# Kernel optimization log

Measured on AMD Instinct MI355X. Metric: run time of the kernel, lower is better.

## Reference

```python
import jax, jax.numpy as jnp
import numpy as np

B, NNODE, FIN, FOUT = 64, 512, 64, 64

def setup_inputs() -> dict:
    key = jax.random.key(0)
    ks = jax.random.split(key, 8)
    stdW = 1.0 / np.sqrt(FIN)
    stdA = 1.0 / np.sqrt(FOUT)
    return {
        "X": jax.random.normal(ks[0], (B, NNODE, FIN), dtype=jnp.float32),
        "A": jax.random.uniform(ks[1], (B, NNODE, NNODE), dtype=jnp.float32),
        "N": jax.random.randint(ks[2], (B,), 1, NNODE + 1, dtype=jnp.int64),
        "W": jax.random.uniform(ks[3], (FIN, FOUT), jnp.float32, -stdW, stdW),
        "a": jax.random.uniform(ks[4], (FOUT, FOUT), jnp.float32, -stdA, stdA),
        "bias_W": jax.random.uniform(ks[5], (FOUT,), jnp.float32, -stdW, stdW),
        "bias_a": jax.random.uniform(ks[6], (NNODE,), jnp.float32, -1.0 / np.sqrt(NNODE), 1.0 / np.sqrt(NNODE)),
    }

def reference(X, A, N, W, a, bias_W, bias_a):
    # A_ = A + identity on the top-left n_atoms block (only diagonal entries)
    idx = jnp.arange(A.shape[1])
    diag_mask = (idx[None, :] < N[:, None]).astype(A.dtype)  # [B, n]
    A_ = A + jnp.einsum('bn,nm->bnm', diag_mask, jnp.eye(A.shape[1], dtype=A.dtype))
    # XW: [B, n, F_out]
    XW = jnp.einsum('bnc,cd->bnd', X, W)
    # buf[a,j,k] = sum_i a[i,j] * XW^T[a,j,k]  (einsum 'ij,ajk->ajk')
    col_sum = a.sum(axis=0)  # [F_out]
    XWT = jnp.swapaxes(XW, 1, 2)  # [B, F_out, n]
    buf = col_sum[None, :, None] * XWT
    Z = jnp.einsum('bif,bfk->bik', XW, buf) + bias_a  # [B, n, n] + [n] broadcast on last dim
    att = jnp.tanh(jnp.einsum('bij,bjk->bik', A_, Z))
    H = jnp.einsum('bij,bjd->bid', att, XW) + bias_W
    return H
```

## Files before the change

### kernel.cpp

```cpp
#include <hip/hip_runtime.h>

#define BB 64
#define NN 512
#define FD 64

typedef short bf16x8 __attribute__((ext_vector_type(8)));
typedef float f32x4 __attribute__((ext_vector_type(4)));

__device__ __forceinline__ unsigned short f2bf(float f){
    unsigned u = __builtin_bit_cast(unsigned, f);
    u += 0x7fffu + ((u >> 16) & 1u);
    return (unsigned short)(u >> 16);
}
__device__ __forceinline__ float bf2f(unsigned short h){
    unsigned u = ((unsigned)h) << 16;
    return __builtin_bit_cast(float, u);
}
__device__ __forceinline__ float fast_tanh(float x){
    float e = __expf(2.0f * x);
    return 1.0f - 2.0f * __builtin_amdgcn_rcpf(e + 1.0f);
}
__device__ __forceinline__ bf16x8 pack8(float4 a, float4 b){
    bf16x8 r;
    r[0]=(short)f2bf(a.x); r[1]=(short)f2bf(a.y); r[2]=(short)f2bf(a.z); r[3]=(short)f2bf(a.w);
    r[4]=(short)f2bf(b.x); r[5]=(short)f2bf(b.y); r[6]=(short)f2bf(b.z); r[7]=(short)f2bf(b.w);
    return r;
}

__global__ __launch_bounds__(256) void k_xw(const float* __restrict__ X,
                                            const float* __restrict__ W,
                                            const float* __restrict__ a,
                                            float* __restrict__ colsum,
                                            unsigned short* __restrict__ XWh,
                                            unsigned short* __restrict__ XWt){
    __shared__ float Wf[64][68];
    __shared__ float cpart[4][64];
    __shared__ unsigned short Xl[64][72];
    __shared__ unsigned short Wtl[64][72];
    __shared__ unsigned short Cl[64][72];
    __shared__ unsigned short ClT[64][72];
    int t = threadIdx.x;
    int row0 = blockIdx.x * 64;
    int r = t >> 2, c0 = (t & 3) * 16;
    {
        const float4* srcW = (const float4*)&W[r*64 + c0];
        #pragma unroll
        for (int q = 0; q < 4; q++) *(float4*)&Wf[r][c0 + q*4] = srcW[q];
        const float4* srcX = (const float4*)&X[(row0 + r)*FD + c0];
        #pragma unroll
        for (int q = 0; q < 4; q++){
            float4 v = srcX[q];
            ushort4 h; h.x=f2bf(v.x); h.y=f2bf(v.y); h.z=f2bf(v.z); h.w=f2bf(v.w);
            *(ushort4*)&Xl[r][c0 + q*4] = h;
        }
    }
    if (blockIdx.x == 0){
        int d = t & 63, part = t >> 6;
        float s = 0.f;
        #pragma unroll
        for (int i = 0; i < 16; i++) s += a[(part*16 + i)*64 + d];
        cpart[part][d] = s;
    }
    __syncthreads();
    #pragma unroll
    for (int q = 0; q < 4; q++){
        ushort4 o;
        #pragma unroll
        for (int jj = 0; jj < 4; jj++)
            ((unsigned short*)&o)[jj] = f2bf(Wf[c0 + q*4 + jj][r]);
        *(ushort4*)&Wtl[r][c0 + q*4] = o;
    }
    if (blockIdx.x == 0 && t < 64)
        colsum[t] = cpart[0][t] + cpart[1][t] + cpart[2][t] + cpart[3][t];
    __syncthreads();
    int lane = t & 63, w = t >> 6, l15 = lane & 15, quad = lane >> 4;
    f32x4 acc[4] = {{0,0,0,0},{0,0,0,0},{0,0,0,0},{0,0,0,0}};
    #pragma unroll
    for (int ks = 0; ks < 2; ks++){
        bf16x8 af = *(const bf16x8*)&Xl[w*16 + l15][ks*32 + quad*8];
        #pragma unroll
        for (int nt = 0; nt < 4; nt++){
            bf16x8 bfr = *(const bf16x8*)&Wtl[nt*16 + l15][ks*32 + quad*8];
            acc[nt] = __builtin_amdgcn_mfma_f32_16x16x32_bf16(af, bfr, acc[nt], 0, 0, 0);
        }
    }
    #pragma unroll
    for (int nt = 0; nt < 4; nt++)
        #pragma unroll
        for (int rg = 0; rg < 4; rg++){
            unsigned short hb = f2bf(acc[nt][rg]);
            Cl [w*16 + quad*4 + rg][nt*16 + l15] = hb;
            ClT[nt*16 + l15][w*16 + quad*4 + rg] = hb;
        }
    __syncthreads();
    int b = blockIdx.x >> 3, n0 = (blockIdx.x & 7) * 64;
    {
        uint4 v0 = *(const uint4*)&Cl[r][c0];
        uint4 v1 = *(const uint4*)&Cl[r][c0 + 8];
        *(uint4*)&XWh[(row0 + r)*FD + c0]     = v0;
        *(uint4*)&XWh[(row0 + r)*FD + c0 + 8] = v1;
    }
    {
        uint4 v0 = *(const uint4*)&ClT[r][c0];
        uint4 v1 = *(const uint4*)&ClT[r][c0 + 8];
        *(uint4*)&XWt[(b*64 + r)*NN + n0 + c0]     = v0;
        *(uint4*)&XWt[(b*64 + r)*NN + n0 + c0 + 8] = v1;
    }
}

__global__ __launch_bounds__(512, 2) void k_fused(const float* __restrict__ A,
                                               const unsigned short* __restrict__ XWh,
                                               const unsigned short* __restrict__ XWt,
                                               const float* __restrict__ colsum,
                                               const int* __restrict__ Ni,
                                               const float* __restrict__ bias_a,
                                               const float* __restrict__ bias_W,
                                               float* __restrict__ H){
    __shared__ unsigned short XWtL[64][516];
    __shared__ unsigned short XWhL[512][68];
    __shared__ unsigned short P[2][64][72];
    __shared__ float bl[512];
    __shared__ float csl[64];
    __shared__ float rsl[64];
    int t = threadIdx.x;
    int b = blockIdx.x, it = blockIdx.y;
    int i0 = it * 64;
    int Nb = (Ni[1] == 0) ? Ni[2*b] : Ni[b];
    int lane = t & 63, w = t >> 6, l15 = lane & 15, quad = lane >> 4;
    int wr = w & 3, wc = w >> 2;
    const unsigned short* XWtb = XWt + b*64*NN;
    const unsigned short* XWhb = XWh + b*NN*FD;
    const float* Arow = A + (size_t)(b*NN + i0 + wr*16 + l15)*NN + quad*8;

    #pragma unroll
    for (int q = 0; q < 8; q++){
        int m = t + 512*q;
        *(uint4*)&XWtL[m >> 6][(m & 63)*8] = *(const uint4*)&XWtb[(m >> 6)*NN + (m & 63)*8];
    }
    #pragma unroll
    for (int q = 0; q < 8; q++){
        int m = t + 512*q;
        *(uint4*)&XWhL[m >> 3][(m & 7)*8] = *(const uint4*)&XWhb[(m >> 3)*FD + (m & 7)*8];
    }
    bl[t] = bias_a[t];
    if (t < 64) csl[t] = colsum[t];
    __syncthreads();

    f32x4 acc[2] = {{0,0,0,0},{0,0,0,0}};
    float rs = 0.f;
    #pragma unroll
    for (int c = 0; c < 8; c++){
        bf16x8 af[2];
        #pragma unroll
        for (int ks = 0; ks < 2; ks++){
            float4 v0 = *(const float4*)&Arow[c*64 + ks*32];
            float4 v1 = *(const float4*)&Arow[c*64 + ks*32 + 4];
            rs += (v0.x + v0.y) + (v0.z + v0.w) + (v1.x + v1.y) + (v1.z + v1.w);
            af[ks] = pack8(v0, v1);
        }
        #pragma unroll
        for (int ks = 0; ks < 2; ks++)
            #pragma unroll
            for (int nt = 0; nt < 2; nt++){
                bf16x8 bfr = *(const bf16x8*)&XWtL[wc*32 + nt*16 + l15][c*64 + ks*32 + quad*8];
                acc[nt] = __builtin_amdgcn_mfma_f32_16x16x32_bf16(af[ks], bfr, acc[nt], 0, 0, 0);
            }
    }
    #pragma unroll
    for (int nt = 0; nt < 2; nt++)
        #pragma unroll
        for (int rg = 0; rg < 4; rg++){
            int i = i0 + wr*16 + quad*4 + rg;
            if (i < Nb) acc[nt][rg] += bf2f(XWhL[i][wc*32 + nt*16 + l15]);
        }
    if (wc == 0){
        float r1 = rs + __shfl_xor(rs, 16);
        float r2 = r1 + __shfl_xor(r1, 32);
        if (lane < 16) rsl[wr*16 + lane] = r2;
    }
    #pragma unroll
    for (int nt = 0; nt < 2; nt++){
        float cs = csl[wc*32 + nt*16 + l15];
        #pragma unroll
        for (int rg = 0; rg < 4; rg++)
            P[0][wr*16 + quad*4 + rg][wc*32 + nt*16 + l15] = f2bf(acc[nt][rg] * cs);
    }
    __syncthreads();
    bf16x8 maf[2];
    maf[0] = *(const bf16x8*)&P[0][wr*16 + l15][quad*8];
    maf[1] = *(const bf16x8*)&P[0][wr*16 + l15][32 + quad*8];
    float rs_r[4];
    #pragma unroll
    for (int rg = 0; rg < 4; rg++){
        int i = i0 + wr*16 + quad*4 + rg;
        rs_r[rg] = rsl[wr*16 + quad*4 + rg] + ((i < Nb) ? 1.f : 0.f);
    }

    f32x4 hacc[2] = {{0,0,0,0},{0,0,0,0}};
    #pragma unroll
    for (int jt = 0; jt < 8; jt++){
        int pb = (jt + 1) & 1;
        #pragma unroll
        for (int nt = 0; nt < 2; nt++){
            float bv = bl[jt*64 + wc*32 + nt*16 + l15];
            f32x4 arg = { rs_r[0]*bv, rs_r[1]*bv, rs_r[2]*bv, rs_r[3]*bv };
            #pragma unroll
            for (int ks = 0; ks < 2; ks++){
                bf16x8 bfr = *(const bf16x8*)&XWhL[jt*64 + wc*32 + nt*16 + l15][ks*32 + quad*8];
                arg = __builtin_amdgcn_mfma_f32_16x16x32_bf16(maf[ks], bfr, arg, 0, 0, 0);
            }
            #pragma unroll
            for (int rg = 0; rg < 4; rg++)
                P[pb][wr*16 + quad*4 + rg][wc*32 + nt*16 + l15] = f2bf(fast_tanh(arg[rg]));
        }
        __syncthreads();
        #pragma unroll
        for (int ks = 0; ks < 2; ks++){
            bf16x8 paf = *(const bf16x8*)&P[pb][wr*16 + l15][ks*32 + quad*8];
            #pragma unroll
            for (int dt = 0; dt < 2; dt++){
                bf16x8 bfr = *(const bf16x8*)&XWtL[wc*32 + dt*16 + l15][jt*64 + ks*32 + quad*8];
                hacc[dt] = __builtin_amdgcn_mfma_f32_16x16x32_bf16(paf, bfr, hacc[dt], 0, 0, 0);
            }
        }
    }
    #pragma unroll
    for (int dt = 0; dt < 2; dt++){
        float bw = bias_W[wc*32 + dt*16 + l15];
        #pragma unroll
        for (int rg = 0; rg < 4; rg++)
            H[(size_t)(b*NN + i0 + wr*16 + quad*4 + rg)*FD + wc*32 + dt*16 + l15] = hacc[dt][rg] + bw;
    }
}

extern "C" void kernel_launch(void* const* d_in, const int* in_sizes, int n_in,
                              void* d_out, int out_size, void* d_ws, size_t ws_size,
                              hipStream_t stream){
    const float* X      = (const float*)d_in[0];
    const float* A      = (const float*)d_in[1];
    const int*   N      = (const int*)  d_in[2];
    const float* W      = (const float*)d_in[3];
    const float* a      = (const float*)d_in[4];
    const float* bias_W = (const float*)d_in[5];
    const float* bias_a = (const float*)d_in[6];
    float* H = (float*)d_out;
    char* ws = (char*)d_ws;

    unsigned short* XWh    = (unsigned short*)(ws);
    unsigned short* XWt    = (unsigned short*)(ws + (4u<<20));
    float*          colsum = (float*)(ws + (8u<<20));

    k_xw   <<<BB * NN / 64, 256, 0, stream>>>(X, W, a, colsum, XWh, XWt);
    k_fused<<<dim3(BB, 8), 512, 0, stream>>>(A, XWh, XWt, colsum, N, bias_a, bias_W, H);
}
```

Before: 136.2 us.

## Give each wave a full 16-row strip to drop block barriers in fused kernel

Each wave now owns a complete 16-row by 64-column output strip, and each block covers two 64-row tiles, which halves the grid to 256 blocks. With no data shared between waves, the per-iteration __syncthreads calls are replaced by per-wave LDS scratch and lgkmcnt waits, and row sums are exchanged with shuffles instead of shared memory. A rows are prefetched into registers four steps ahead, and LDS padding is changed. The cost is higher register pressure (launch bounds relaxed to one block per CU), fewer blocks, and a larger share of the XW staging per block.

```diff
diff --git a/kernel.cpp b/kernel.cpp
--- a/kernel.cpp
+++ b/kernel.cpp
@@ -108,7 +108,7 @@
     }
 }
 
-__global__ __launch_bounds__(512, 2) void k_fused(const float* __restrict__ A,
+__global__ __launch_bounds__(512, 1) void k_fused(const float* __restrict__ A,
                                                const unsigned short* __restrict__ XWh,
                                                const unsigned short* __restrict__ XWt,
                                                const float* __restrict__ colsum,
@@ -116,22 +116,27 @@
                                                const float* __restrict__ bias_a,
                                                const float* __restrict__ bias_W,
                                                float* __restrict__ H){
-    __shared__ unsigned short XWtL[64][516];
-    __shared__ unsigned short XWhL[512][68];
-    __shared__ unsigned short P[2][64][72];
+    __shared__ unsigned short XWtL[64][520];
+    __shared__ unsigned short XWhL[512][72];
+    __shared__ unsigned short Pl[8][16][72];
     __shared__ float bl[512];
     __shared__ float csl[64];
-    __shared__ float rsl[64];
     int t = threadIdx.x;
-    int b = blockIdx.x, it = blockIdx.y;
-    int i0 = it * 64;
+    int b = blockIdx.x, it2 = blockIdx.y;
+    int lane = t & 63, w = t >> 6, l15 = lane & 15, quad = lane >> 4;
+    int tl = w >> 2, st = w & 3;
+    int i0 = (it2 + 4*tl) * 64;
     int Nb = (Ni[1] == 0) ? Ni[2*b] : Ni[b];
-    int lane = t & 63, w = t >> 6, l15 = lane & 15, quad = lane >> 4;
-    int wr = w & 3, wc = w >> 2;
     const unsigned short* XWtb = XWt + b*64*NN;
     const unsigned short* XWhb = XWh + b*NN*FD;
-    const float* Arow = A + (size_t)(b*NN + i0 + wr*16 + l15)*NN + quad*8;
-
+    const float* Arow = A + (size_t)(b*NN + i0 + st*16 + l15)*NN + quad*8;
+
+    float4 pa[4][2];
+    #pragma unroll
+    for (int s = 0; s < 4; s++){
+        pa[s][0] = *(const float4*)&Arow[s*32];
+        pa[s][1] = *(const float4*)&Arow[s*32 + 4];
+    }
     #pragma unroll
     for (int q = 0; q < 8; q++){
         int m = t + 512*q;
@@ -146,90 +151,86 @@
     if (t < 64) csl[t] = colsum[t];
     __syncthreads();
 
-    f32x4 acc[2] = {{0,0,0,0},{0,0,0,0}};
+    f32x4 acc[4] = {{0,0,0,0},{0,0,0,0},{0,0,0,0},{0,0,0,0}};
     float rs = 0.f;
     #pragma unroll
-    for (int c = 0; c < 8; c++){
-        bf16x8 af[2];
-        #pragma unroll
-        for (int ks = 0; ks < 2; ks++){
-            float4 v0 = *(const float4*)&Arow[c*64 + ks*32];
-            float4 v1 = *(const float4*)&Arow[c*64 + ks*32 + 4];
-            rs += (v0.x + v0.y) + (v0.z + v0.w) + (v1.x + v1.y) + (v1.z + v1.w);
-            af[ks] = pack8(v0, v1);
-        }
-        #pragma unroll
-        for (int ks = 0; ks < 2; ks++)
-            #pragma unroll
-            for (int nt = 0; nt < 2; nt++){
-                bf16x8 bfr = *(const bf16x8*)&XWtL[wc*32 + nt*16 + l15][c*64 + ks*32 + quad*8];
-                acc[nt] = __builtin_amdgcn_mfma_f32_16x16x32_bf16(af[ks], bfr, acc[nt], 0, 0, 0);
-            }
-    }
-    #pragma unroll
-    for (int nt = 0; nt < 2; nt++)
+    for (int s = 0; s < 16; s++){
+        float4 v0 = pa[s & 3][0], v1 = pa[s & 3][1];
+        if (s < 12){
+            pa[s & 3][0] = *(const float4*)&Arow[(s + 4)*32];
+            pa[s & 3][1] = *(const float4*)&Arow[(s + 4)*32 + 4];
+        }
+        rs += (v0.x + v0.y) + (v0.z + v0.w) + (v1.x + v1.y) + (v1.z + v1.w);
+        bf16x8 af = pack8(v0, v1);
+        #pragma unroll
+        for (int nt = 0; nt < 4; nt++){
+            bf16x8 bfr = *(const bf16x8*)&XWtL[nt*16 + l15][s*32 + quad*8];
+            acc[nt] = __builtin_amdgcn_mfma_f32_16x16x32_bf16(af, bfr, acc[nt], 0, 0, 0);
+        }
+    }
+    #pragma unroll
+    for (int nt = 0; nt < 4; nt++)
         #pragma unroll
         for (int rg = 0; rg < 4; rg++){
-            int i = i0 + wr*16 + quad*4 + rg;
-            if (i < Nb) acc[nt][rg] += bf2f(XWhL[i][wc*32 + nt*16 + l15]);
-        }
-    if (wc == 0){
-        float r1 = rs + __shfl_xor(rs, 16);
-        float r2 = r1 + __shfl_xor(r1, 32);
-        if (lane < 16) rsl[wr*16 + lane] = r2;
-    }
-    #pragma unroll
-    for (int nt = 0; nt < 2; nt++){
-        float cs = csl[wc*32 + nt*16 + l15];
+            int i = i0 + st*16 + quad*4 + rg;
+            if (i < Nb) acc[nt][rg] += bf2f(XWhL[i][nt*16 + l15]);
+        }
+    float rsum = rs;
+    rsum += __shfl_xor(rsum, 16);
+    rsum += __shfl_xor(rsum, 32);
+    #pragma unroll
+    for (int nt = 0; nt < 4; nt++){
+        float cs = csl[nt*16 + l15];
         #pragma unroll
         for (int rg = 0; rg < 4; rg++)
-            P[0][wr*16 + quad*4 + rg][wc*32 + nt*16 + l15] = f2bf(acc[nt][rg] * cs);
-    }
-    __syncthreads();
+            Pl[w][quad*4 + rg][nt*16 + l15] = f2bf(acc[nt][rg] * cs);
+    }
+    asm volatile("s_waitcnt lgkmcnt(0)" ::: "memory");
+    __builtin_amdgcn_sched_barrier(0);
     bf16x8 maf[2];
-    maf[0] = *(const bf16x8*)&P[0][wr*16 + l15][quad*8];
-    maf[1] = *(const bf16x8*)&P[0][wr*16 + l15][32 + quad*8];
+    maf[0] = *(const bf16x8*)&Pl[w][l15][quad*8];
+    maf[1] = *(const bf16x8*)&Pl[w][l15][32 + quad*8];
     float rs_r[4];
     #pragma unroll
     for (int rg = 0; rg < 4; rg++){
-        int i = i0 + wr*16 + quad*4 + rg;
-        rs_r[rg] = rsl[wr*16 + quad*4 + rg] + ((i < Nb) ? 1.f : 0.f);
-    }
-
-    f32x4 hacc[2] = {{0,0,0,0},{0,0,0,0}};
+        int i = i0 + st*16 + quad*4 + rg;
+        rs_r[rg] = __shfl(rsum, quad*4 + rg) + ((i < Nb) ? 1.f : 0.f);
+    }
+
+    f32x4 hacc[4] = {{0,0,0,0},{0,0,0,0},{0,0,0,0},{0,0,0,0}};
     #pragma unroll
     for (int jt = 0; jt < 8; jt++){
-        int pb = (jt + 1) & 1;
-        #pragma unroll
-        for (int nt = 0; nt < 2; nt++){
-            float bv = bl[jt*64 + wc*32 + nt*16 + l15];
+        #pragma unroll
+        for (int nt = 0; nt < 4; nt++){
+            float bv = bl[jt*64 + nt*16 + l15];
             f32x4 arg = { rs_r[0]*bv, rs_r[1]*bv, rs_r[2]*bv, rs_r[3]*bv };
             #pragma unroll
             for (int ks = 0; ks < 2; ks++){
-                bf16x8 bfr = *(const bf16x8*)&XWhL[jt*64 + wc*32 + nt*16 + l15][ks*32 + quad*8];
+                bf16x8 bfr = *(const bf16x8*)&XWhL[jt*64 + nt*16 + l15][ks*32 + quad*8];
                 arg = __builtin_amdgcn_mfma_f32_16x16x32_bf16(maf[ks], bfr, arg, 0, 0, 0);
             }
             #pragma unroll
             for (int rg = 0; rg < 4; rg++)
-                P[pb][wr*16 + quad*4 + rg][wc*32 + nt*16 + l15] = f2bf(fast_tanh(arg[rg]));
-        }
-        __syncthreads();
+                Pl[w][quad*4 + rg][nt*16 + l15] = f2bf(fast_tanh(arg[rg]));
+        }
+        asm volatile("s_waitcnt lgkmcnt(0)" ::: "memory");
+        __builtin_amdgcn_sched_barrier(0);
         #pragma unroll
         for (int ks = 0; ks < 2; ks++){
-            bf16x8 paf = *(const bf16x8*)&P[pb][wr*16 + l15][ks*32 + quad*8];
+            bf16x8 paf = *(const bf16x8*)&Pl[w][l15][ks*32 + quad*8];
             #pragma unroll
-            for (int dt = 0; dt < 2; dt++){
-                bf16x8 bfr = *(const bf16x8*)&XWtL[wc*32 + dt*16 + l15][jt*64 + ks*32 + quad*8];
+            for (int dt = 0; dt < 4; dt++){
+                bf16x8 bfr = *(const bf16x8*)&XWtL[dt*16 + l15][jt*64 + ks*32 + quad*8];
                 hacc[dt] = __builtin_amdgcn_mfma_f32_16x16x32_bf16(paf, bfr, hacc[dt], 0, 0, 0);
             }
         }
     }
     #pragma unroll
-    for (int dt = 0; dt < 2; dt++){
-        float bw = bias_W[wc*32 + dt*16 + l15];
+    for (int dt = 0; dt < 4; dt++){
+        float bw = bias_W[dt*16 + l15];
         #pragma unroll
         for (int rg = 0; rg < 4; rg++)
-            H[(size_t)(b*NN + i0 + wr*16 + quad*4 + rg)*FD + wc*32 + dt*16 + l15] = hacc[dt][rg] + bw;
+            H[(size_t)(b*NN + i0 + st*16 + quad*4 + rg)*FD + dt*16 + l15] = hacc[dt][rg] + bw;
     }
 }
 
@@ -251,5 +252,5 @@
     float*          colsum = (float*)(ws + (8u<<20));
 
     k_xw   <<<BB * NN / 64, 256, 0, stream>>>(X, W, a, colsum, XWh, XWt);
-    k_fused<<<dim3(BB, 8), 512, 0, stream>>>(A, XWh, XWt, colsum, N, bias_a, bias_W, H);
-}
+    k_fused<<<dim3(BB, 4), 512, 0, stream>>>(A, XWh, XWt, colsum, N, bias_a, bias_W, H);
+}
```

New measurement: 128.0 us. -6.0%, faster.
